# Optimization experiments

Measured on AMD Instinct MI355X. Metric: run time of the kernel, lower is better.

The kernel has to match this reference:

```python
import jax, jax.numpy as jnp
import numpy as np

N_NODES = 100000
N_EDGES = 3200000
D = 32


def setup_inputs() -> dict:
    key = jax.random.key(0)
    k = jax.random.split(key, 5)
    x = jax.random.normal(k[0], (N_NODES, D), dtype=jnp.float32)
    edge_index = jax.random.randint(k[1], (2, N_EDGES), 0, N_NODES, dtype=jnp.int64)
    W1 = jax.random.normal(k[2], (D, D), dtype=jnp.float32) * (1.0 / np.sqrt(D))
    b1 = jnp.zeros((D,), dtype=jnp.float32)
    W2 = jax.random.normal(k[3], (D, D), dtype=jnp.float32) * (1.0 / np.sqrt(D))
    b2 = jnp.zeros((D,), dtype=jnp.float32)
    return {"x": x, "edge_index": edge_index, "W1": W1, "b1": b1, "W2": W2, "b2": b2}


def reference(x, edge_index, W1, b1, W2, b2):
    n = x.shape[0]
    # add self-loops (PyG GCNConv default)
    loop = jnp.arange(n, dtype=edge_index.dtype)
    src = jnp.concatenate([edge_index[0], loop])
    dst = jnp.concatenate([edge_index[1], loop])
    # symmetric normalization: deg computed on dst with self-loops; deg >= 1 so no inf handling needed
    deg = jax.ops.segment_sum(jnp.ones_like(src, dtype=x.dtype), dst, num_segments=n)
    dinv = jax.lax.rsqrt(deg)
    norm = (dinv[src] * dinv[dst])[:, None]  # [E+N, 1]

    def gcn_layer(h, W, b):
        h = h @ W.T                                        # dense transform [N, D]
        msg = h[src] * norm                                # gather + scale   [E+N, D]
        agg = jax.ops.segment_sum(msg, dst, num_segments=n)  # scatter-add  [N, D]
        return jax.nn.relu(agg + b)

    h = gcn_layer(x, W1, b1)
    h = gcn_layer(h, W2, b2)
    return h
```

## Files before the change

### kernel.cpp

```cpp
#include <hip/hip_runtime.h>

#define THREADS 256
#define BIGT 1024
#define NBLK 256
#define BSHIFT 8
#define BSZ (1 << BSHIFT)
#define MAXB 512

__global__ void detect_kernel(const unsigned int* ei_words, int* flag_int64, long long n_words) {
    __shared__ int nonzero;
    if (threadIdx.x == 0) nonzero = 0;
    __syncthreads();
    long long w = 2LL * threadIdx.x + 1;
    if (w < n_words) {
        if (ei_words[w] != 0u) atomicOr(&nonzero, 1);
    }
    __syncthreads();
    if (threadIdx.x == 0) *flag_int64 = (nonzero == 0) ? 1 : 0;
}

__global__ __launch_bounds__(BIGT) void bin_count_kernel(
        const void* __restrict__ ei, const int* __restrict__ flag_int64,
        int* __restrict__ blockhist, int E, int NB) {
    __shared__ int h[MAXB];
    int tid = threadIdx.x;
    for (int i = tid; i < NB; i += blockDim.x) h[i] = 0;
    __syncthreads();
    int chunk = (E + gridDim.x - 1) / gridDim.x;
    int s = blockIdx.x * chunk;
    int e = min(E, s + chunk);
    if (*flag_int64) {
        const long long* p = (const long long*)ei;
        for (int i = s + tid; i < e; i += blockDim.x)
            atomicAdd(&h[(int)p[E + i] >> BSHIFT], 1);
    } else {
        const int* p = (const int*)ei;
        for (int i = s + tid; i < e; i += blockDim.x)
            atomicAdd(&h[p[E + i] >> BSHIFT], 1);
    }
    __syncthreads();
    for (int i = tid; i < NB; i += blockDim.x)
        blockhist[i * NBLK + blockIdx.x] = h[i];
}

__global__ __launch_bounds__(BIGT) void bin_write_kernel(
        const void* __restrict__ ei, const int* __restrict__ flag_int64,
        const int* __restrict__ offsets, unsigned int* __restrict__ ebuf,
        int E, int NB) {
    __shared__ int cur[MAXB];
    int tid = threadIdx.x;
    for (int i = tid; i < NB; i += blockDim.x)
        cur[i] = offsets[i * NBLK + blockIdx.x];
    __syncthreads();
    int chunk = (E + gridDim.x - 1) / gridDim.x;
    int s = blockIdx.x * chunk;
    int e = min(E, s + chunk);
    if (*flag_int64) {
        const long long* p = (const long long*)ei;
        for (int i = s + tid; i < e; i += blockDim.x) {
            int d = (int)p[E + i];
            int sr = (int)p[i];
            int pos = atomicAdd(&cur[d >> BSHIFT], 1);
            ebuf[pos] = ((unsigned int)(d & (BSZ - 1)) << 20) | (unsigned int)sr;
        }
    } else {
        const int* p = (const int*)ei;
        for (int i = s + tid; i < e; i += blockDim.x) {
            int d = p[E + i];
            int sr = p[i];
            int pos = atomicAdd(&cur[d >> BSHIFT], 1);
            ebuf[pos] = ((unsigned int)(d & (BSZ - 1)) << 20) | (unsigned int)sr;
        }
    }
}

__global__ void scan_blocks_kernel(const int* __restrict__ cnt, int* __restrict__ ofs,
                                   int* __restrict__ partials, int T) {
    __shared__ int sd[THREADS];
    int tid = threadIdx.x;
    int base = blockIdx.x * 1024 + tid * 4;
    int c0 = (base + 0 < T) ? cnt[base + 0] : 0;
    int c1 = (base + 1 < T) ? cnt[base + 1] : 0;
    int c2 = (base + 2 < T) ? cnt[base + 2] : 0;
    int c3 = (base + 3 < T) ? cnt[base + 3] : 0;
    int tsum = c0 + c1 + c2 + c3;
    sd[tid] = tsum;
    __syncthreads();
    for (int off = 1; off < THREADS; off <<= 1) {
        int t = (tid >= off) ? sd[tid - off] : 0;
        __syncthreads();
        sd[tid] += t;
        __syncthreads();
    }
    int excl = sd[tid] - tsum;
    if (base + 0 < T) ofs[base + 0] = excl;
    if (base + 1 < T) ofs[base + 1] = excl + c0;
    if (base + 2 < T) ofs[base + 2] = excl + c0 + c1;
    if (base + 3 < T) ofs[base + 3] = excl + c0 + c1 + c2;
    if (tid == THREADS - 1) partials[blockIdx.x] = sd[tid];
}

__global__ void scan_add2_kernel(int* __restrict__ ofs, const int* __restrict__ partials,
                                 int T, int SB) {
    __shared__ int sd[128];
    int tid = threadIdx.x;
    if (tid < 128) sd[tid] = (tid < SB) ? partials[tid] : 0;
    __syncthreads();
    for (int off = 1; off < 128; off <<= 1) {
        int t = (tid < 128 && tid >= off) ? sd[tid - off] : 0;
        __syncthreads();
        if (tid < 128) sd[tid] += t;
        __syncthreads();
    }
    int add = (blockIdx.x > 0) ? sd[blockIdx.x - 1] : 0;
    int base = blockIdx.x * 1024 + tid * 4;
    if (base + 0 < T) ofs[base + 0] += add;
    if (base + 1 < T) ofs[base + 1] += add;
    if (base + 2 < T) ofs[base + 2] += add;
    if (base + 3 < T) ofs[base + 3] += add;
    if (blockIdx.x == gridDim.x - 1 && tid == 0) ofs[T] = sd[SB - 1];
}

__global__ __launch_bounds__(BIGT) void place_dense_kernel(
        const unsigned int* __restrict__ ebuf, const int* __restrict__ offsets,
        const float* __restrict__ x, const float* __restrict__ W1,
        int* __restrict__ rowptr, float* __restrict__ dinv, int* __restrict__ col,
        float* __restrict__ ht1, int N, int NB) {
    __shared__ int cnt[BSZ];
    __shared__ int scanbuf[BSZ];
    __shared__ int baseL[BSZ];
    __shared__ int fillL[BSZ];
    __shared__ float dinvL[BSZ];
    __shared__ float Wt[1024];
    __shared__ float xs[BIGT];
    int b = blockIdx.x;
    int lo = b << BSHIFT;
    int tid = threadIdx.x;
    if (tid < BSZ) cnt[tid] = 0;
    Wt[(tid & 31) * 32 + (tid >> 5)] = W1[tid];
    __syncthreads();
    int start = offsets[b * NBLK];
    int end   = offsets[(b + 1) * NBLK];
    for (int p = start + tid; p < end; p += BIGT)
        atomicAdd(&cnt[(ebuf[p] >> 20) & (BSZ - 1)], 1);
    __syncthreads();
    int c = (tid < BSZ) ? cnt[tid] : 0;
    if (tid < BSZ) scanbuf[tid] = c;
    __syncthreads();
    for (int off = 1; off < BSZ; off <<= 1) {
        int t = (tid < BSZ && tid >= off) ? scanbuf[tid - off] : 0;
        __syncthreads();
        if (tid < BSZ) scanbuf[tid] += t;
        __syncthreads();
    }
    if (tid < BSZ) {
        int excl = scanbuf[tid] - c;
        int node = lo + tid;
        float dv = 1.0f / sqrtf((float)(c + 1));
        dinvL[tid] = dv;
        if (node < N) {
            rowptr[node] = start + excl;
            dinv[node] = dv;
            if (node == N - 1) rowptr[N] = start + excl + c;
        }
        baseL[tid] = start + excl;
        fillL[tid] = 0;
    }
    __syncthreads();
    for (int p = start + tid; p < end; p += BIGT) {
        unsigned int v = ebuf[p];
        int dl = (v >> 20) & (BSZ - 1);
        int pos = baseL[dl] + atomicAdd(&fillL[dl], 1);
        col[pos] = (int)(v & 0xFFFFFu);
    }
    __syncthreads();
    for (int base0 = 0; base0 < BSZ * 32; base0 += BIGT) {
        int idx = base0 + tid;
        int ln = idx >> 5;
        int node = lo + ln;
        xs[tid] = (node < N) ? x[(size_t)lo * 32 + idx] : 0.f;
        __syncthreads();
        if (node < N) {
            int j = idx & 31;
            const float* xr = xs + ((tid >> 5) << 5);
            float s = 0.f;
#pragma unroll
            for (int k = 0; k < 32; ++k) s = fmaf(xr[k], Wt[k * 32 + j], s);
            ht1[(size_t)node * 32 + j] = s * dinvL[ln];
        }
        __syncthreads();
    }
}

__global__ __launch_bounds__(THREADS) void agg_dense_kernel(
        const float* __restrict__ ht1, const int* __restrict__ rowptr,
        const int* __restrict__ col, const float* __restrict__ dinv,
        const float* __restrict__ b1, const float* __restrict__ W2,
        float* __restrict__ ht2, int N) {
    __shared__ float Wt[1024];
    __shared__ float hr[THREADS];
    int tid = threadIdx.x;
    for (int idx = tid; idx < 1024; idx += THREADS)
        Wt[(idx & 31) * 32 + (idx >> 5)] = W2[idx];
    int gid = blockIdx.x * THREADS + tid;
    int n = gid >> 5;
    int j = gid & 31;
    bool act = (n < N);
    float h1v = 0.f, dv = 0.f;
    if (act) {
        dv = dinv[n];
        float s = ht1[gid];
        int p = rowptr[n], end = rowptr[n + 1];
        for (; p + 8 <= end; p += 8) {
            int c0 = col[p], c1 = col[p + 1], c2 = col[p + 2], c3 = col[p + 3];
            int c4 = col[p + 4], c5 = col[p + 5], c6 = col[p + 6], c7 = col[p + 7];
            float v0 = ht1[c0 * 32 + j];
            float v1 = ht1[c1 * 32 + j];
            float v2 = ht1[c2 * 32 + j];
            float v3 = ht1[c3 * 32 + j];
            float v4 = ht1[c4 * 32 + j];
            float v5 = ht1[c5 * 32 + j];
            float v6 = ht1[c6 * 32 + j];
            float v7 = ht1[c7 * 32 + j];
            s += ((v0 + v1) + (v2 + v3)) + ((v4 + v5) + (v6 + v7));
        }
        for (; p + 4 <= end; p += 4) {
            int c0 = col[p], c1 = col[p + 1], c2 = col[p + 2], c3 = col[p + 3];
            float v0 = ht1[c0 * 32 + j];
            float v1 = ht1[c1 * 32 + j];
            float v2 = ht1[c2 * 32 + j];
            float v3 = ht1[c3 * 32 + j];
            s += (v0 + v1) + (v2 + v3);
        }
        for (; p < end; ++p) s += ht1[col[p] * 32 + j];
        h1v = fmaxf(fmaf(dv, s, b1[j]), 0.f);
    }
    hr[tid] = h1v;
    __syncthreads();
    if (act) {
        const float* hrow = hr + ((tid >> 5) << 5);
        float t = 0.f;
#pragma unroll
        for (int k = 0; k < 32; ++k) t = fmaf(hrow[k], Wt[k * 32 + j], t);
        ht2[gid] = t * dv;
    }
}

__global__ __launch_bounds__(THREADS) void agg_final_kernel(
        const float* __restrict__ ht2, const int* __restrict__ rowptr,
        const int* __restrict__ col, const float* __restrict__ dinv,
        const float* __restrict__ bias, float* __restrict__ out, int N) {
    int gid = blockIdx.x * THREADS + threadIdx.x;
    int n = gid >> 5;
    if (n >= N) return;
    int j = gid & 31;
    float s = ht2[gid];
    int p = rowptr[n], end = rowptr[n + 1];
    for (; p + 8 <= end; p += 8) {
        int c0 = col[p], c1 = col[p + 1], c2 = col[p + 2], c3 = col[p + 3];
        int c4 = col[p + 4], c5 = col[p + 5], c6 = col[p + 6], c7 = col[p + 7];
        float v0 = ht2[c0 * 32 + j];
        float v1 = ht2[c1 * 32 + j];
        float v2 = ht2[c2 * 32 + j];
        float v3 = ht2[c3 * 32 + j];
        float v4 = ht2[c4 * 32 + j];
        float v5 = ht2[c5 * 32 + j];
        float v6 = ht2[c6 * 32 + j];
        float v7 = ht2[c7 * 32 + j];
        s += ((v0 + v1) + (v2 + v3)) + ((v4 + v5) + (v6 + v7));
    }
    for (; p + 4 <= end; p += 4) {
        int c0 = col[p], c1 = col[p + 1], c2 = col[p + 2], c3 = col[p + 3];
        float v0 = ht2[c0 * 32 + j];
        float v1 = ht2[c1 * 32 + j];
        float v2 = ht2[c2 * 32 + j];
        float v3 = ht2[c3 * 32 + j];
        s += (v0 + v1) + (v2 + v3);
    }
    for (; p < end; ++p) s += ht2[col[p] * 32 + j];
    out[gid] = fmaxf(fmaf(dinv[n], s, bias[j]), 0.f);
}

extern "C" void kernel_launch(void* const* d_in, const int* in_sizes, int n_in,
                              void* d_out, int out_size, void* d_ws, size_t ws_size,
                              hipStream_t stream) {
    const float* x  = (const float*)d_in[0];
    const void*  ei = d_in[1];
    const float* W1 = (const float*)d_in[2];
    const float* b1 = (const float*)d_in[3];
    const float* W2 = (const float*)d_in[4];
    const float* b2 = (const float*)d_in[5];
    float* out = (float*)d_out;

    int N = in_sizes[0] / 32;
    long long twoE = (long long)in_sizes[1];
    int E = (int)(twoE / 2);
    int NB = (N + BSZ - 1) >> BSHIFT;
    int T  = NB * NBLK;

    char* ws = (char*)d_ws;
    size_t o = 0;
    auto alloc = [&](size_t bytes) { size_t r = o; o += (bytes + 255) & ~(size_t)255; return r; };
    int*   flag      = (int*)(ws + alloc(4));
    int*   blockhist = (int*)(ws + alloc((size_t)T * 4));
    int*   offsets   = (int*)(ws + alloc((size_t)(T + 1) * 4));
    int*   rowptr    = (int*)(ws + alloc((size_t)(N + 1) * 4));
    int*   partials  = (int*)(ws + alloc(512));
    float* dinv      = (float*)(ws + alloc((size_t)N * 4));
    unsigned int* ebuf = (unsigned int*)(ws + alloc((size_t)E * 4));
    int*   col       = (int*)(ws + alloc((size_t)E * 4));
    float* ht1       = (float*)(ws + alloc((size_t)N * 32 * 4));
    float* ht2       = (float*)(ws + alloc((size_t)N * 32 * 4));

    detect_kernel<<<1, 256, 0, stream>>>((const unsigned int*)ei, flag, twoE);

    bin_count_kernel<<<NBLK, BIGT, 0, stream>>>(ei, flag, blockhist, E, NB);

    int SB = (T + 1023) / 1024;
    scan_blocks_kernel<<<SB, THREADS, 0, stream>>>(blockhist, offsets, partials, T);
    scan_add2_kernel<<<SB, THREADS, 0, stream>>>(offsets, partials, T, SB);

    bin_write_kernel<<<NBLK, BIGT, 0, stream>>>(ei, flag, offsets, ebuf, E, NB);
    place_dense_kernel<<<NB, BIGT, 0, stream>>>(ebuf, offsets, x, W1, rowptr, dinv, col, ht1, N, NB);

    int GB = (N * 32 + THREADS - 1) / THREADS;
    agg_dense_kernel<<<GB, THREADS, 0, stream>>>(ht1, rowptr, col, dinv, b1, W2, ht2, N);
    agg_final_kernel<<<GB, THREADS, 0, stream>>>(ht2, rowptr, col, dinv, b2, out, N);
}
```

Baseline: 272.8 us.

## Sub-sort CSR neighbors by source tile and keep weight rows in registers

The place kernel now buckets each destination's edges into 8 sub-bins by high bits of the source index, so neighbor lists come out roughly sorted by source region. This should improve cache locality of the gather loads in the aggregation kernels. Separately, the 32x32 weight matrices move from shared memory into per-thread register arrays, and the padded shared row buffers avoid bank conflicts. The cost is more shared-memory histogram bins, an extra per-node prefix step, and higher register pressure that may reduce occupancy.

```diff
diff --git a/kernel.cpp b/kernel.cpp
--- a/kernel.cpp
+++ b/kernel.cpp
@@ -6,6 +6,8 @@
 #define BSHIFT 8
 #define BSZ (1 << BSHIFT)
 #define MAXB 512
+#define TSHIFT 14
+#define NT 8
 
 __global__ void detect_kernel(const unsigned int* ei_words, int* flag_int64, long long n_words) {
     __shared__ int nonzero;
@@ -126,67 +128,82 @@
         const float* __restrict__ x, const float* __restrict__ W1,
         int* __restrict__ rowptr, float* __restrict__ dinv, int* __restrict__ col,
         float* __restrict__ ht1, int N, int NB) {
-    __shared__ int cnt[BSZ];
+    __shared__ int base2[BSZ * NT];
+    __shared__ int fill2[BSZ * NT];
     __shared__ int scanbuf[BSZ];
-    __shared__ int baseL[BSZ];
-    __shared__ int fillL[BSZ];
     __shared__ float dinvL[BSZ];
-    __shared__ float Wt[1024];
-    __shared__ float xs[BIGT];
+    __shared__ float xs[32 * 33];
     int b = blockIdx.x;
     int lo = b << BSHIFT;
     int tid = threadIdx.x;
-    if (tid < BSZ) cnt[tid] = 0;
-    Wt[(tid & 31) * 32 + (tid >> 5)] = W1[tid];
+    int j0 = tid & 31;
+    float w1r[32];
+#pragma unroll
+    for (int k = 0; k < 32; ++k) w1r[k] = W1[j0 * 32 + k];
+    for (int i = tid; i < BSZ * NT; i += BIGT) base2[i] = 0;
     __syncthreads();
     int start = offsets[b * NBLK];
     int end   = offsets[(b + 1) * NBLK];
-    for (int p = start + tid; p < end; p += BIGT)
-        atomicAdd(&cnt[(ebuf[p] >> 20) & (BSZ - 1)], 1);
-    __syncthreads();
-    int c = (tid < BSZ) ? cnt[tid] : 0;
-    if (tid < BSZ) scanbuf[tid] = c;
-    __syncthreads();
-    for (int off = 1; off < BSZ; off <<= 1) {
-        int t = (tid < BSZ && tid >= off) ? scanbuf[tid - off] : 0;
-        __syncthreads();
-        if (tid < BSZ) scanbuf[tid] += t;
-        __syncthreads();
-    }
-    if (tid < BSZ) {
-        int excl = scanbuf[tid] - c;
-        int node = lo + tid;
-        float dv = 1.0f / sqrtf((float)(c + 1));
-        dinvL[tid] = dv;
-        if (node < N) {
-            rowptr[node] = start + excl;
-            dinv[node] = dv;
-            if (node == N - 1) rowptr[N] = start + excl + c;
-        }
-        baseL[tid] = start + excl;
-        fillL[tid] = 0;
-    }
-    __syncthreads();
     for (int p = start + tid; p < end; p += BIGT) {
         unsigned int v = ebuf[p];
         int dl = (v >> 20) & (BSZ - 1);
-        int pos = baseL[dl] + atomicAdd(&fillL[dl], 1);
-        col[pos] = (int)(v & 0xFFFFFu);
+        int t  = ((v & 0xFFFFFu) >> TSHIFT) & (NT - 1);
+        atomicAdd(&base2[dl * NT + t], 1);
+    }
+    __syncthreads();
+    int ctot = 0;
+    int pre[NT];
+    if (tid < BSZ) {
+#pragma unroll
+        for (int t = 0; t < NT; ++t) { pre[t] = ctot; ctot += base2[tid * NT + t]; }
+        scanbuf[tid] = ctot;
+    }
+    __syncthreads();
+    for (int off = 1; off < BSZ; off <<= 1) {
+        int t = (tid < BSZ && tid >= off) ? scanbuf[tid - off] : 0;
+        __syncthreads();
+        if (tid < BSZ) scanbuf[tid] += t;
+        __syncthreads();
+    }
+    if (tid < BSZ) {
+        int excl = scanbuf[tid] - ctot;
+        int nodebase = start + excl;
+        int node = lo + tid;
+        float dv = 1.0f / sqrtf((float)(ctot + 1));
+        dinvL[tid] = dv;
+        if (node < N) {
+            rowptr[node] = nodebase;
+            dinv[node] = dv;
+            if (node == N - 1) rowptr[N] = nodebase + ctot;
+        }
+#pragma unroll
+        for (int t = 0; t < NT; ++t) {
+            base2[tid * NT + t] = nodebase + pre[t];
+            fill2[tid * NT + t] = 0;
+        }
+    }
+    __syncthreads();
+    for (int p = start + tid; p < end; p += BIGT) {
+        unsigned int v = ebuf[p];
+        int dl = (v >> 20) & (BSZ - 1);
+        int sr = (int)(v & 0xFFFFFu);
+        int idx2 = dl * NT + ((sr >> TSHIFT) & (NT - 1));
+        int pos = base2[idx2] + atomicAdd(&fill2[idx2], 1);
+        col[pos] = sr;
     }
     __syncthreads();
     for (int base0 = 0; base0 < BSZ * 32; base0 += BIGT) {
         int idx = base0 + tid;
         int ln = idx >> 5;
         int node = lo + ln;
-        xs[tid] = (node < N) ? x[(size_t)lo * 32 + idx] : 0.f;
+        int g = tid >> 5;
+        xs[g * 33 + j0] = (node < N) ? x[(size_t)lo * 32 + idx] : 0.f;
         __syncthreads();
         if (node < N) {
-            int j = idx & 31;
-            const float* xr = xs + ((tid >> 5) << 5);
             float s = 0.f;
 #pragma unroll
-            for (int k = 0; k < 32; ++k) s = fmaf(xr[k], Wt[k * 32 + j], s);
-            ht1[(size_t)node * 32 + j] = s * dinvL[ln];
+            for (int k = 0; k < 32; ++k) s = fmaf(xs[g * 33 + k], w1r[k], s);
+            ht1[(size_t)lo * 32 + idx] = s * dinvL[ln];
         }
         __syncthreads();
     }
@@ -197,14 +214,15 @@
         const int* __restrict__ col, const float* __restrict__ dinv,
         const float* __restrict__ b1, const float* __restrict__ W2,
         float* __restrict__ ht2, int N) {
-    __shared__ float Wt[1024];
-    __shared__ float hr[THREADS];
-    int tid = threadIdx.x;
-    for (int idx = tid; idx < 1024; idx += THREADS)
-        Wt[(idx & 31) * 32 + (idx >> 5)] = W2[idx];
+    __shared__ float hr[8 * 33];
+    int tid = threadIdx.x;
+    int j = tid & 31;
+    int g = tid >> 5;
+    float w2r[32];
+#pragma unroll
+    for (int k = 0; k < 32; ++k) w2r[k] = W2[j * 32 + k];
     int gid = blockIdx.x * THREADS + tid;
     int n = gid >> 5;
-    int j = gid & 31;
     bool act = (n < N);
     float h1v = 0.f, dv = 0.f;
     if (act) {
@@ -235,13 +253,12 @@
         for (; p < end; ++p) s += ht1[col[p] * 32 + j];
         h1v = fmaxf(fmaf(dv, s, b1[j]), 0.f);
     }
-    hr[tid] = h1v;
+    hr[g * 33 + j] = h1v;
     __syncthreads();
     if (act) {
-        const float* hrow = hr + ((tid >> 5) << 5);
         float t = 0.f;
 #pragma unroll
-        for (int k = 0; k < 32; ++k) t = fmaf(hrow[k], Wt[k * 32 + j], t);
+        for (int k = 0; k < 32; ++k) t = fmaf(hr[g * 33 + k], w2r[k], t);
         ht2[gid] = t * dv;
     }
 }
```

Result: slower. 312.6 us (+14.6%).
